# Kernel tuning notes

Hardware: AMD Instinct MI355X
Metric: run time of the kernel (lower is better)

## Reference

```python
import jax, jax.numpy as jnp
import numpy as np

B_SZ, L, D, N = 2, 2048, 1024, 16


def setup_inputs() -> dict:
    key = jax.random.key(0)
    ks = jax.random.split(key, 8)
    x = jax.random.normal(ks[0], (B_SZ, L, D), dtype=jnp.float32)
    # torch.nn.Linear params: weight [out, in], bias [out]; y = x @ W.T + b
    s1 = 1.0 / np.sqrt(D)
    W1 = jax.random.uniform(ks[1], (D, D), minval=-s1, maxval=s1, dtype=jnp.float32)
    b1 = jax.random.uniform(ks[2], (D,), minval=-s1, maxval=s1, dtype=jnp.float32)
    W2 = jax.random.uniform(ks[3], (N, D), minval=-s1, maxval=s1, dtype=jnp.float32)
    b2 = jax.random.uniform(ks[4], (N,), minval=-s1, maxval=s1, dtype=jnp.float32)
    W3 = jax.random.uniform(ks[5], (N, D), minval=-s1, maxval=s1, dtype=jnp.float32)
    b3 = jax.random.uniform(ks[6], (N,), minval=-s1, maxval=s1, dtype=jnp.float32)
    # A: xavier_uniform on (D, N)
    lim = np.sqrt(6.0 / (D + N))
    A = jax.random.uniform(ks[7], (D, N), minval=-lim, maxval=lim, dtype=jnp.float32)
    return {"x": x, "W1": W1, "b1": b1, "W2": W2, "b2": b2, "W3": W3, "b3": b3, "A": A}


def reference(x, W1, b1, W2, b2, W3, b3, A):
    # delta = softplus(fc1(x)); B = fc2(x); C = fc3(x)
    delta = jax.nn.softplus(x @ W1.T + b1)          # [b, l, d]
    Bm = x @ W2.T + b2                               # [b, l, n]
    Cm = x @ W3.T + b3                               # [b, l, n]
    # discretization: dB = einsum('bld,bln->bldn', delta, B)
    dB = jnp.einsum('bld,bln->bldn', delta, Bm)      # [b, l, d, n]
    # dA = exp(einsum('bld,dn->bldn', delta, A)) is computed in the source but
    # multiplies a zero-initialized h, so it does not affect the output.
    # h = dA*0 + x[..., None] * dB
    h = x[..., None] * dB                            # [b, l, d, n]
    y = jnp.einsum('bln,bldn->bld', Cm, h)           # [b, l, d]
    return y
```

## Files before the change

kernel.cpp:

```cpp
#include <hip/hip_runtime.h>
#include <hip/hip_bf16.h>
#include <math.h>


typedef __bf16 bf16x8 __attribute__((ext_vector_type(8)));
typedef __bf16 bf16x4 __attribute__((ext_vector_type(4)));
typedef float  f32x4  __attribute__((ext_vector_type(4)));

#define MDIM 4096
#define KDIM 1024
#define NDIM 1024

__device__ __forceinline__ void async16(const void* g, void* l) {
    __builtin_amdgcn_global_load_lds(
        (const __attribute__((address_space(1))) void*)g,
        (__attribute__((address_space(3))) void*)l, 16, 0, 0);
}

__device__ __forceinline__ float softplus_f(float z) {
    return fmaxf(z, 0.f) + log1pf(__expf(-fabsf(z)));
}

__global__ __launch_bounds__(256)
void prep_kernel(const float* __restrict__ x, const float* __restrict__ W1,
                 const float* __restrict__ W2, const float* __restrict__ b2,
                 const float* __restrict__ W3, const float* __restrict__ b3,
                 __bf16* __restrict__ xb, __bf16* __restrict__ w1b,
                 float* __restrict__ s) {
    __shared__ __align__(16) __bf16 xs[16 * 1032];
    __shared__ float red[4][2][16][16];
    const int t = threadIdx.x;
    const int wave = t >> 6, lane = t & 63;
    const int lrow = lane & 15, quad = lane >> 4;
    const size_t m0 = (size_t)blockIdx.x * 16;

    {
        const float4* src = reinterpret_cast<const float4*>(W1) + (size_t)blockIdx.x * 1024;
        bf16x4* dst = reinterpret_cast<bf16x4*>(w1b) + (size_t)blockIdx.x * 1024;
#pragma unroll
        for (int i = 0; i < 4; ++i) {
            float4 v = src[i * 256 + t];
            bf16x4 h = { (__bf16)v.x, (__bf16)v.y, (__bf16)v.z, (__bf16)v.w };
            dst[i * 256 + t] = h;
        }
    }

#pragma unroll
    for (int i = 0; i < 16; ++i) {
        float4 v = *reinterpret_cast<const float4*>(x + (m0 + i) * KDIM + t * 4);
        bf16x4 h = { (__bf16)v.x, (__bf16)v.y, (__bf16)v.z, (__bf16)v.w };
        *reinterpret_cast<bf16x4*>(&xs[i * 1032 + t * 4]) = h;
        *reinterpret_cast<bf16x4*>(xb + (m0 + i) * KDIM + t * 4) = h;
    }
    __syncthreads();

    f32x4 acc[2] = {};
    const int wk0 = wave * 256;
#pragma unroll
    for (int ks = 0; ks < 256; ks += 32) {
        bf16x8 a = *reinterpret_cast<const bf16x8*>(
            &xs[lrow * 1032 + wk0 + ks + quad * 8]);
        {
            const float* wp = W2 + (size_t)lrow * KDIM + wk0 + ks + quad * 8;
            float4 v0 = *reinterpret_cast<const float4*>(wp);
            float4 v1 = *reinterpret_cast<const float4*>(wp + 4);
            bf16x8 b = { (__bf16)v0.x, (__bf16)v0.y, (__bf16)v0.z, (__bf16)v0.w,
                         (__bf16)v1.x, (__bf16)v1.y, (__bf16)v1.z, (__bf16)v1.w };
            acc[0] = __builtin_amdgcn_mfma_f32_16x16x32_bf16(a, b, acc[0], 0, 0, 0);
        }
        {
            const float* wp = W3 + (size_t)lrow * KDIM + wk0 + ks + quad * 8;
            float4 v0 = *reinterpret_cast<const float4*>(wp);
            float4 v1 = *reinterpret_cast<const float4*>(wp + 4);
            bf16x8 b = { (__bf16)v0.x, (__bf16)v0.y, (__bf16)v0.z, (__bf16)v0.w,
                         (__bf16)v1.x, (__bf16)v1.y, (__bf16)v1.z, (__bf16)v1.w };
            acc[1] = __builtin_amdgcn_mfma_f32_16x16x32_bf16(a, b, acc[1], 0, 0, 0);
        }
    }
#pragma unroll
    for (int r = 0; r < 4; ++r) {
        red[wave][0][quad * 4 + r][lrow] = acc[0][r];
        red[wave][1][quad * 4 + r][lrow] = acc[1][r];
    }
    __syncthreads();

    {
        const int row = t >> 4, n = t & 15;
        float Bv = red[0][0][row][n] + red[1][0][row][n]
                 + red[2][0][row][n] + red[3][0][row][n] + b2[n];
        float Cv = red[0][1][row][n] + red[1][1][row][n]
                 + red[2][1][row][n] + red[3][1][row][n] + b3[n];
        float p = Bv * Cv;
        p += __shfl_xor(p, 1);
        p += __shfl_xor(p, 2);
        p += __shfl_xor(p, 4);
        p += __shfl_xor(p, 8);
        if (n == 0) s[m0 + row] = p;
    }
}

#define GBM 128
#define GBN 64
#define GBK 64
__global__ __launch_bounds__(256)
void gemm_bf(const __bf16* __restrict__ xb, const __bf16* __restrict__ w1b,
             const float* __restrict__ x, const float* __restrict__ b1,
             const float* __restrict__ s, float* __restrict__ y) {
    __shared__ __align__(16) __bf16 As[GBM * GBK];
    __shared__ __align__(16) __bf16 Bs[GBN * GBK];
    const int bm = blockIdx.y, bn = blockIdx.x;
    const int t = threadIdx.x;
    const int wave = t >> 6, lane = t & 63;
    const int wm = (wave >> 1) * 64, wn = (wave & 1) * 32;
    const int lrow = lane & 15, quad = lane >> 4;
    const int srow = lane >> 3;
    const int scol = ((lane & 7) ^ srow) * 8;
    const size_t m0 = (size_t)bm * GBM, n0 = (size_t)bn * GBN;

    f32x4 acc[4][2] = {};

    for (int k0 = 0; k0 < KDIM; k0 += GBK) {
#pragma unroll
        for (int i = 0; i < 4; ++i) {
            int q = i * 4 + wave;
            int row = 8 * q + srow;
            async16(xb + (m0 + row) * KDIM + k0 + scol, &As[q * 512]);
        }
#pragma unroll
        for (int i = 0; i < 2; ++i) {
            int q = i * 4 + wave;
            int row = 8 * q + srow;
            async16(w1b + (n0 + row) * KDIM + k0 + scol, &Bs[q * 512]);
        }
        __syncthreads();

#pragma unroll
        for (int kk = 0; kk < GBK; kk += 32) {
            const int cg = (kk >> 3) + quad;
            bf16x8 af[4], bfr[2];
#pragma unroll
            for (int mi = 0; mi < 4; ++mi) {
                int row = wm + mi * 16 + lrow;
                af[mi] = *reinterpret_cast<const bf16x8*>(
                    &As[row * 64 + ((cg ^ (row & 7)) << 3)]);
            }
#pragma unroll
            for (int ni = 0; ni < 2; ++ni) {
                int row = wn + ni * 16 + lrow;
                bfr[ni] = *reinterpret_cast<const bf16x8*>(
                    &Bs[row * 64 + ((cg ^ (row & 7)) << 3)]);
            }
#pragma unroll
            for (int mi = 0; mi < 4; ++mi)
#pragma unroll
                for (int ni = 0; ni < 2; ++ni)
                    acc[mi][ni] = __builtin_amdgcn_mfma_f32_16x16x32_bf16(
                        af[mi], bfr[ni], acc[mi][ni], 0, 0, 0);
        }
        __syncthreads();
    }

#pragma unroll
    for (int ni = 0; ni < 2; ++ni) {
        const size_t gn = n0 + wn + ni * 16 + lrow;
        const float bias = b1[gn];
#pragma unroll
        for (int mi = 0; mi < 4; ++mi) {
#pragma unroll
            for (int r = 0; r < 4; ++r) {
                const size_t gm = m0 + wm + mi * 16 + quad * 4 + r;
                float z = acc[mi][ni][r] + bias;
                y[gm * NDIM + gn] = x[gm * NDIM + gn] * softplus_f(z) * s[gm];
            }
        }
    }
}

__global__ __launch_bounds__(256)
void s_kernel_fb(const float* __restrict__ x,
                 const float* __restrict__ W2, const float* __restrict__ b2,
                 const float* __restrict__ W3, const float* __restrict__ b3,
                 float* __restrict__ s) {
    __shared__ float xs[1024];
    __shared__ float ps[8][32];
    __shared__ float bc[32];
    const int m = blockIdx.x;
    const int t = threadIdx.x;
    reinterpret_cast<float4*>(xs)[t] =
        reinterpret_cast<const float4*>(x + (size_t)m * 1024)[t];
    __syncthreads();
    const int n = t & 15;
    const int mat = (t >> 4) & 1;
    const int seg = t >> 5;
    const float* __restrict__ W = mat ? W3 : W2;
    const float* __restrict__ wr = W + (size_t)n * 1024 + seg * 128;
    const float* __restrict__ xr = xs + seg * 128;
    float p = 0.f;
#pragma unroll
    for (int i = 0; i < 128; i += 4) {
        float4 w4 = *reinterpret_cast<const float4*>(wr + i);
        float4 x4 = *reinterpret_cast<const float4*>(xr + i);
        p += w4.x * x4.x + w4.y * x4.y + w4.z * x4.z + w4.w * x4.w;
    }
    ps[seg][t & 31] = p;
    __syncthreads();
    if (t < 32) {
        float tot = 0.f;
#pragma unroll
        for (int g = 0; g < 8; ++g) tot += ps[g][t];
        tot += (t < 16) ? b2[t] : b3[t - 16];
        bc[t] = tot;
    }
    __syncthreads();
    if (t == 0) {
        float ss = 0.f;
#pragma unroll
        for (int nn = 0; nn < 16; ++nn) ss += bc[nn] * bc[16 + nn];
        s[m] = ss;
    }
}

#define BM 128
#define BN 64
#define BK 64
#define LDK 72
__global__ __launch_bounds__(256)
void gemm_fused_fb(const float* __restrict__ x, const float* __restrict__ W1,
                   const float* __restrict__ b1, const float* __restrict__ s,
                   float* __restrict__ y) {
    __shared__ __align__(16) __bf16 As[BM * LDK];
    __shared__ __align__(16) __bf16 Bs[BN * LDK];
    const int bm = blockIdx.y;
    const int bn = blockIdx.x;
    const int t = threadIdx.x;
    const int wave = t >> 6;
    const int lane = t & 63;
    const int wm = (wave >> 1) * 64;
    const int wn = (wave & 1) * 32;
    const int lrow = lane & 15;
    const int quad = lane >> 4;
    f32x4 acc[4][2] = {};
    const int rbase = t >> 4;
    const int scol = (t & 15) * 4;
    const float* __restrict__ xg = x + (size_t)(bm * BM) * KDIM + scol;
    const float* __restrict__ wg = W1 + (size_t)(bn * BN) * KDIM + scol;
    for (int k0 = 0; k0 < KDIM; k0 += BK) {
#pragma unroll
        for (int rr = 0; rr < 8; ++rr) {
            int row = rr * 16 + rbase;
            float4 v = *reinterpret_cast<const float4*>(xg + (size_t)row * KDIM + k0);
            bf16x4 h = { (__bf16)v.x, (__bf16)v.y, (__bf16)v.z, (__bf16)v.w };
            *reinterpret_cast<bf16x4*>(&As[row * LDK + scol]) = h;
        }
#pragma unroll
        for (int rr = 0; rr < 4; ++rr) {
            int row = rr * 16 + rbase;
            float4 v = *reinterpret_cast<const float4*>(wg + (size_t)row * KDIM + k0);
            bf16x4 h = { (__bf16)v.x, (__bf16)v.y, (__bf16)v.z, (__bf16)v.w };
            *reinterpret_cast<bf16x4*>(&Bs[row * LDK + scol]) = h;
        }
        __syncthreads();
#pragma unroll
        for (int kk = 0; kk < BK; kk += 32) {
            bf16x8 af[4];
            bf16x8 bfr[2];
#pragma unroll
            for (int mi = 0; mi < 4; ++mi)
                af[mi] = *reinterpret_cast<const bf16x8*>(
                    &As[(wm + mi * 16 + lrow) * LDK + kk + quad * 8]);
#pragma unroll
            for (int ni = 0; ni < 2; ++ni)
                bfr[ni] = *reinterpret_cast<const bf16x8*>(
                    &Bs[(wn + ni * 16 + lrow) * LDK + kk + quad * 8]);
#pragma unroll
            for (int mi = 0; mi < 4; ++mi)
#pragma unroll
                for (int ni = 0; ni < 2; ++ni)
                    acc[mi][ni] = __builtin_amdgcn_mfma_f32_16x16x32_bf16(
                        af[mi], bfr[ni], acc[mi][ni], 0, 0, 0);
        }
        __syncthreads();
    }
    const int gmb = bm * BM + wm;
    const int gnb = bn * BN + wn;
#pragma unroll
    for (int ni = 0; ni < 2; ++ni) {
        const int gn = gnb + ni * 16 + lrow;
        const float bias = b1[gn];
#pragma unroll
        for (int mi = 0; mi < 4; ++mi) {
            const int gm0 = gmb + mi * 16 + quad * 4;
#pragma unroll
            for (int r = 0; r < 4; ++r) {
                const int gm = gm0 + r;
                float z = acc[mi][ni][r] + bias;
                y[(size_t)gm * NDIM + gn] =
                    x[(size_t)gm * NDIM + gn] * softplus_f(z) * s[gm];
            }
        }
    }
}

extern "C" void kernel_launch(void* const* d_in, const int* in_sizes, int n_in,
                              void* d_out, int out_size, void* d_ws, size_t ws_size,
                              hipStream_t stream) {
    const float* x  = (const float*)d_in[0];
    const float* W1 = (const float*)d_in[1];
    const float* b1 = (const float*)d_in[2];
    const float* W2 = (const float*)d_in[3];
    const float* b2 = (const float*)d_in[4];
    const float* W3 = (const float*)d_in[5];
    const float* b3 = (const float*)d_in[6];

    float* y = (float*)d_out;

    const size_t XB_BYTES = (size_t)MDIM * KDIM * 2;
    const size_t WB_BYTES = (size_t)NDIM * KDIM * 2;
    const size_t S_BYTES  = (size_t)MDIM * 4;

    if (ws_size >= XB_BYTES + WB_BYTES + S_BYTES) {
        __bf16* xb  = (__bf16*)d_ws;
        __bf16* w1b = (__bf16*)((char*)d_ws + XB_BYTES);
        float*  s   = (float*)((char*)d_ws + XB_BYTES + WB_BYTES);
        prep_kernel<<<dim3(MDIM / 16), dim3(256), 0, stream>>>(
            x, W1, W2, b2, W3, b3, xb, w1b, s);
        gemm_bf<<<dim3(NDIM / GBN, MDIM / GBM), dim3(256), 0, stream>>>(
            xb, w1b, x, b1, s, y);
    } else {
        float* s = (float*)d_ws;
        s_kernel_fb<<<dim3(MDIM), dim3(256), 0, stream>>>(x, W2, b2, W3, b3, s);
        gemm_fused_fb<<<dim3(NDIM / BN, MDIM / BM), dim3(256), 0, stream>>>(x, W1, b1, s, y);
    }
}
```

Baseline: 114.0 us.

## Stage W2/W3 in LDS for prep; double GEMM K tile and set occupancy hint

In the prep kernel, each wave now loads and converts its slice of W2 and W3 into a padded LDS buffer once, before the MFMA loop. Previously those fp32 weights were fetched and converted inline for every k-step. The GEMM's K tile grows from 64 to 128, which halves the number of barrier-separated iterations, and its XOR swizzle widens to 16 column groups. Launch bounds now request 2 blocks per CU. This raises LDS use per block (about 48KB in the GEMM, plus a large prep buffer) and has no pipelining, so occupancy may drop.

```diff
diff --git a/kernel.cpp b/kernel.cpp
--- a/kernel.cpp
+++ b/kernel.cpp
@@ -28,11 +28,13 @@
                  __bf16* __restrict__ xb, __bf16* __restrict__ w1b,
                  float* __restrict__ s) {
     __shared__ __align__(16) __bf16 xs[16 * 1032];
+    __shared__ __align__(16) __bf16 wq[4][32 * 264];
     __shared__ float red[4][2][16][16];
     const int t = threadIdx.x;
     const int wave = t >> 6, lane = t & 63;
     const int lrow = lane & 15, quad = lane >> 4;
     const size_t m0 = (size_t)blockIdx.x * 16;
+    const int wk0 = wave * 256;
 
     {
         const float4* src = reinterpret_cast<const float4*>(W1) + (size_t)blockIdx.x * 1024;
@@ -52,30 +54,40 @@
         *reinterpret_cast<bf16x4*>(&xs[i * 1032 + t * 4]) = h;
         *reinterpret_cast<bf16x4*>(xb + (m0 + i) * KDIM + t * 4) = h;
     }
+
+    {
+        const int r16  = lane >> 2;
+        const int cseg = (lane & 3) * 64;
+#pragma unroll
+        for (int j = 0; j < 8; ++j) {
+            const int col = cseg + j * 8;
+            const float* p2 = W2 + (size_t)r16 * KDIM + wk0 + col;
+            float4 a0 = *reinterpret_cast<const float4*>(p2);
+            float4 a1 = *reinterpret_cast<const float4*>(p2 + 4);
+            bf16x8 h2 = { (__bf16)a0.x, (__bf16)a0.y, (__bf16)a0.z, (__bf16)a0.w,
+                          (__bf16)a1.x, (__bf16)a1.y, (__bf16)a1.z, (__bf16)a1.w };
+            *reinterpret_cast<bf16x8*>(&wq[wave][r16 * 264 + col]) = h2;
+            const float* p3 = W3 + (size_t)r16 * KDIM + wk0 + col;
+            float4 c0 = *reinterpret_cast<const float4*>(p3);
+            float4 c1 = *reinterpret_cast<const float4*>(p3 + 4);
+            bf16x8 h3 = { (__bf16)c0.x, (__bf16)c0.y, (__bf16)c0.z, (__bf16)c0.w,
+                          (__bf16)c1.x, (__bf16)c1.y, (__bf16)c1.z, (__bf16)c1.w };
+            *reinterpret_cast<bf16x8*>(&wq[wave][(16 + r16) * 264 + col]) = h3;
+        }
+    }
     __syncthreads();
 
     f32x4 acc[2] = {};
-    const int wk0 = wave * 256;
 #pragma unroll
     for (int ks = 0; ks < 256; ks += 32) {
         bf16x8 a = *reinterpret_cast<const bf16x8*>(
             &xs[lrow * 1032 + wk0 + ks + quad * 8]);
-        {
-            const float* wp = W2 + (size_t)lrow * KDIM + wk0 + ks + quad * 8;
-            float4 v0 = *reinterpret_cast<const float4*>(wp);
-            float4 v1 = *reinterpret_cast<const float4*>(wp + 4);
-            bf16x8 b = { (__bf16)v0.x, (__bf16)v0.y, (__bf16)v0.z, (__bf16)v0.w,
-                         (__bf16)v1.x, (__bf16)v1.y, (__bf16)v1.z, (__bf16)v1.w };
-            acc[0] = __builtin_amdgcn_mfma_f32_16x16x32_bf16(a, b, acc[0], 0, 0, 0);
-        }
-        {
-            const float* wp = W3 + (size_t)lrow * KDIM + wk0 + ks + quad * 8;
-            float4 v0 = *reinterpret_cast<const float4*>(wp);
-            float4 v1 = *reinterpret_cast<const float4*>(wp + 4);
-            bf16x8 b = { (__bf16)v0.x, (__bf16)v0.y, (__bf16)v0.z, (__bf16)v0.w,
-                         (__bf16)v1.x, (__bf16)v1.y, (__bf16)v1.z, (__bf16)v1.w };
-            acc[1] = __builtin_amdgcn_mfma_f32_16x16x32_bf16(a, b, acc[1], 0, 0, 0);
-        }
+        bf16x8 b0 = *reinterpret_cast<const bf16x8*>(
+            &wq[wave][lrow * 264 + ks + quad * 8]);
+        acc[0] = __builtin_amdgcn_mfma_f32_16x16x32_bf16(a, b0, acc[0], 0, 0, 0);
+        bf16x8 b1 = *reinterpret_cast<const bf16x8*>(
+            &wq[wave][(16 + lrow) * 264 + ks + quad * 8]);
+        acc[1] = __builtin_amdgcn_mfma_f32_16x16x32_bf16(a, b1, acc[1], 0, 0, 0);
     }
 #pragma unroll
     for (int r = 0; r < 4; ++r) {
@@ -101,8 +113,8 @@
 
 #define GBM 128
 #define GBN 64
-#define GBK 64
-__global__ __launch_bounds__(256)
+#define GBK 128
+__global__ __launch_bounds__(256, 2)
 void gemm_bf(const __bf16* __restrict__ xb, const __bf16* __restrict__ w1b,
              const float* __restrict__ x, const float* __restrict__ b1,
              const float* __restrict__ s, float* __restrict__ y) {
@@ -113,24 +125,26 @@
     const int wave = t >> 6, lane = t & 63;
     const int wm = (wave >> 1) * 64, wn = (wave & 1) * 32;
     const int lrow = lane & 15, quad = lane >> 4;
-    const int srow = lane >> 3;
-    const int scol = ((lane & 7) ^ srow) * 8;
+    const int sr  = lane >> 4;
+    const int pcg = lane & 15;
     const size_t m0 = (size_t)bm * GBM, n0 = (size_t)bn * GBN;
 
     f32x4 acc[4][2] = {};
 
     for (int k0 = 0; k0 < KDIM; k0 += GBK) {
+#pragma unroll
+        for (int i = 0; i < 8; ++i) {
+            int q = i * 4 + wave;
+            int row = q * 4 + sr;
+            int lcg = pcg ^ (row & 15);
+            async16(xb + (m0 + row) * KDIM + k0 + lcg * 8, &As[q * 512]);
+        }
 #pragma unroll
         for (int i = 0; i < 4; ++i) {
             int q = i * 4 + wave;
-            int row = 8 * q + srow;
-            async16(xb + (m0 + row) * KDIM + k0 + scol, &As[q * 512]);
-        }
-#pragma unroll
-        for (int i = 0; i < 2; ++i) {
-            int q = i * 4 + wave;
-            int row = 8 * q + srow;
-            async16(w1b + (n0 + row) * KDIM + k0 + scol, &Bs[q * 512]);
+            int row = q * 4 + sr;
+            int lcg = pcg ^ (row & 15);
+            async16(w1b + (n0 + row) * KDIM + k0 + lcg * 8, &Bs[q * 512]);
         }
         __syncthreads();
 
@@ -142,13 +156,13 @@
             for (int mi = 0; mi < 4; ++mi) {
                 int row = wm + mi * 16 + lrow;
                 af[mi] = *reinterpret_cast<const bf16x8*>(
-                    &As[row * 64 + ((cg ^ (row & 7)) << 3)]);
+                    &As[row * GBK + ((cg ^ (row & 15)) << 3)]);
             }
 #pragma unroll
             for (int ni = 0; ni < 2; ++ni) {
                 int row = wn + ni * 16 + lrow;
                 bfr[ni] = *reinterpret_cast<const bf16x8*>(
-                    &Bs[row * 64 + ((cg ^ (row & 7)) << 3)]);
+                    &Bs[row * GBK + ((cg ^ (row & 15)) << 3)]);
             }
 #pragma unroll
             for (int mi = 0; mi < 4; ++mi)
```

Result: no change. 115.2 us (+1.0%).

## Double-buffer GEMM shared tiles and rewrite prep kernel with fp32 row dot products

Applied to the files above, without the earlier changes.

The main GEMM now uses two shared-memory stages. The next K tile is issued asynchronously while the current one is consumed, which removes one barrier per iteration and overlaps global-to-LDS copies with MFMA work. The prep kernel is restructured to handle 4 rows per block instead of 16. It computes the B and C projections as fp32 dot products with wave shuffles rather than bf16 MFMA, which raises parallelism but means each block rereads the W2/W3 rows. Shared memory for the GEMM doubles, which may reduce occupancy.

```diff
diff --git a/kernel.cpp b/kernel.cpp
--- a/kernel.cpp
+++ b/kernel.cpp
@@ -21,93 +21,95 @@
     return fmaxf(z, 0.f) + log1pf(__expf(-fabsf(z)));
 }
 
+__device__ __forceinline__ float dot4(float4 a, float4 b) {
+    return a.x * b.x + a.y * b.y + a.z * b.z + a.w * b.w;
+}
+
 __global__ __launch_bounds__(256)
-void prep_kernel(const float* __restrict__ x, const float* __restrict__ W1,
-                 const float* __restrict__ W2, const float* __restrict__ b2,
-                 const float* __restrict__ W3, const float* __restrict__ b3,
-                 __bf16* __restrict__ xb, __bf16* __restrict__ w1b,
-                 float* __restrict__ s) {
-    __shared__ __align__(16) __bf16 xs[16 * 1032];
-    __shared__ float red[4][2][16][16];
+void convert_s(const float* __restrict__ x, const float* __restrict__ W1,
+               const float* __restrict__ W2, const float* __restrict__ b2,
+               const float* __restrict__ W3, const float* __restrict__ b3,
+               __bf16* __restrict__ xb, __bf16* __restrict__ w1b,
+               float* __restrict__ s) {
+    __shared__ float xs[4][1024];
+    __shared__ float part[32][4];
     const int t = threadIdx.x;
     const int wave = t >> 6, lane = t & 63;
-    const int lrow = lane & 15, quad = lane >> 4;
-    const size_t m0 = (size_t)blockIdx.x * 16;
+    const size_t m0 = (size_t)blockIdx.x * 4;
 
     {
-        const float4* src = reinterpret_cast<const float4*>(W1) + (size_t)blockIdx.x * 1024;
-        bf16x4* dst = reinterpret_cast<bf16x4*>(w1b) + (size_t)blockIdx.x * 1024;
-#pragma unroll
-        for (int i = 0; i < 4; ++i) {
-            float4 v = src[i * 256 + t];
+        const size_t i = (size_t)blockIdx.x * 256 + t;
+        float4 v = reinterpret_cast<const float4*>(W1)[i];
+        bf16x4 h = { (__bf16)v.x, (__bf16)v.y, (__bf16)v.z, (__bf16)v.w };
+        reinterpret_cast<bf16x4*>(w1b)[i] = h;
+    }
+
+    {
+        const float4* src = reinterpret_cast<const float4*>(x + (m0 + wave) * KDIM);
+        bf16x4* dst = reinterpret_cast<bf16x4*>(xb + (m0 + wave) * KDIM);
+#pragma unroll
+        for (int s4 = 0; s4 < 4; ++s4) {
+            float4 v = src[lane + s4 * 64];
             bf16x4 h = { (__bf16)v.x, (__bf16)v.y, (__bf16)v.z, (__bf16)v.w };
-            dst[i * 256 + t] = h;
-        }
-    }
-
-#pragma unroll
-    for (int i = 0; i < 16; ++i) {
-        float4 v = *reinterpret_cast<const float4*>(x + (m0 + i) * KDIM + t * 4);
-        bf16x4 h = { (__bf16)v.x, (__bf16)v.y, (__bf16)v.z, (__bf16)v.w };
-        *reinterpret_cast<bf16x4*>(&xs[i * 1032 + t * 4]) = h;
-        *reinterpret_cast<bf16x4*>(xb + (m0 + i) * KDIM + t * 4) = h;
-    }
-    __syncthreads();
-
-    f32x4 acc[2] = {};
-    const int wk0 = wave * 256;
-#pragma unroll
-    for (int ks = 0; ks < 256; ks += 32) {
-        bf16x8 a = *reinterpret_cast<const bf16x8*>(
-            &xs[lrow * 1032 + wk0 + ks + quad * 8]);
-        {
-            const float* wp = W2 + (size_t)lrow * KDIM + wk0 + ks + quad * 8;
-            float4 v0 = *reinterpret_cast<const float4*>(wp);
-            float4 v1 = *reinterpret_cast<const float4*>(wp + 4);
-            bf16x8 b = { (__bf16)v0.x, (__bf16)v0.y, (__bf16)v0.z, (__bf16)v0.w,
-                         (__bf16)v1.x, (__bf16)v1.y, (__bf16)v1.z, (__bf16)v1.w };
-            acc[0] = __builtin_amdgcn_mfma_f32_16x16x32_bf16(a, b, acc[0], 0, 0, 0);
-        }
-        {
-            const float* wp = W3 + (size_t)lrow * KDIM + wk0 + ks + quad * 8;
-            float4 v0 = *reinterpret_cast<const float4*>(wp);
-            float4 v1 = *reinterpret_cast<const float4*>(wp + 4);
-            bf16x8 b = { (__bf16)v0.x, (__bf16)v0.y, (__bf16)v0.z, (__bf16)v0.w,
-                         (__bf16)v1.x, (__bf16)v1.y, (__bf16)v1.z, (__bf16)v1.w };
-            acc[1] = __builtin_amdgcn_mfma_f32_16x16x32_bf16(a, b, acc[1], 0, 0, 0);
-        }
-    }
-#pragma unroll
-    for (int r = 0; r < 4; ++r) {
-        red[wave][0][quad * 4 + r][lrow] = acc[0][r];
-        red[wave][1][quad * 4 + r][lrow] = acc[1][r];
-    }
-    __syncthreads();
-
-    {
-        const int row = t >> 4, n = t & 15;
-        float Bv = red[0][0][row][n] + red[1][0][row][n]
-                 + red[2][0][row][n] + red[3][0][row][n] + b2[n];
-        float Cv = red[0][1][row][n] + red[1][1][row][n]
-                 + red[2][1][row][n] + red[3][1][row][n] + b3[n];
-        float p = Bv * Cv;
-        p += __shfl_xor(p, 1);
-        p += __shfl_xor(p, 2);
-        p += __shfl_xor(p, 4);
-        p += __shfl_xor(p, 8);
-        if (n == 0) s[m0 + row] = p;
+            dst[lane + s4 * 64] = h;
+            *reinterpret_cast<float4*>(&xs[wave][(lane + s4 * 64) * 4]) = v;
+        }
+    }
+    __syncthreads();
+
+    float4 X[4][4];
+#pragma unroll
+    for (int r = 0; r < 4; ++r)
+#pragma unroll
+        for (int s4 = 0; s4 < 4; ++s4)
+            X[r][s4] = *reinterpret_cast<const float4*>(&xs[r][(lane + s4 * 64) * 4]);
+
+#pragma unroll
+    for (int wr = 0; wr < 8; ++wr) {
+        const int gr = wave * 8 + wr;
+        const float* __restrict__ Wrow = (gr < 16)
+            ? (W2 + (size_t)gr * KDIM) : (W3 + (size_t)(gr - 16) * KDIM);
+        float4 Wv[4];
+#pragma unroll
+        for (int s4 = 0; s4 < 4; ++s4)
+            Wv[s4] = reinterpret_cast<const float4*>(Wrow)[lane + s4 * 64];
+        float p[4];
+#pragma unroll
+        for (int r = 0; r < 4; ++r) {
+            float a = dot4(Wv[0], X[r][0]) + dot4(Wv[1], X[r][1])
+                    + dot4(Wv[2], X[r][2]) + dot4(Wv[3], X[r][3]);
+#pragma unroll
+            for (int d = 1; d < 64; d <<= 1) a += __shfl_xor(a, d);
+            p[r] = a;
+        }
+        if (lane == 0) {
+            part[gr][0] = p[0]; part[gr][1] = p[1];
+            part[gr][2] = p[2]; part[gr][3] = p[3];
+        }
+    }
+    __syncthreads();
+
+    if (t < 64) {
+        const int r = t >> 4, n = t & 15;
+        float v = (part[n][r] + b2[n]) * (part[n + 16][r] + b3[n]);
+        v += __shfl_xor(v, 1);
+        v += __shfl_xor(v, 2);
+        v += __shfl_xor(v, 4);
+        v += __shfl_xor(v, 8);
+        if (n == 0) s[m0 + r] = v;
     }
 }
 
 #define GBM 128
 #define GBN 64
 #define GBK 64
+#define NIT (KDIM / GBK)
 __global__ __launch_bounds__(256)
 void gemm_bf(const __bf16* __restrict__ xb, const __bf16* __restrict__ w1b,
              const float* __restrict__ x, const float* __restrict__ b1,
              const float* __restrict__ s, float* __restrict__ y) {
-    __shared__ __align__(16) __bf16 As[GBM * GBK];
-    __shared__ __align__(16) __bf16 Bs[GBN * GBK];
+    __shared__ __align__(16) __bf16 As[2][GBM * GBK];
+    __shared__ __align__(16) __bf16 Bs[2][GBN * GBK];
     const int bm = blockIdx.y, bn = blockIdx.x;
     const int t = threadIdx.x;
     const int wave = t >> 6, lane = t & 63;
@@ -119,20 +121,34 @@
 
     f32x4 acc[4][2] = {};
 
-    for (int k0 = 0; k0 < KDIM; k0 += GBK) {
-#pragma unroll
-        for (int i = 0; i < 4; ++i) {
-            int q = i * 4 + wave;
-            int row = 8 * q + srow;
-            async16(xb + (m0 + row) * KDIM + k0 + scol, &As[q * 512]);
-        }
-#pragma unroll
-        for (int i = 0; i < 2; ++i) {
-            int q = i * 4 + wave;
-            int row = 8 * q + srow;
-            async16(w1b + (n0 + row) * KDIM + k0 + scol, &Bs[q * 512]);
-        }
+#pragma unroll
+    for (int i = 0; i < 4; ++i) {
+        int q = i * 4 + wave; int row = 8 * q + srow;
+        async16(xb + (m0 + row) * KDIM + scol, &As[0][q * 512]);
+    }
+#pragma unroll
+    for (int i = 0; i < 2; ++i) {
+        int q = i * 4 + wave; int row = 8 * q + srow;
+        async16(w1b + (n0 + row) * KDIM + scol, &Bs[0][q * 512]);
+    }
+
+    for (int it = 0; it < NIT; ++it) {
+        const int p = it & 1;
         __syncthreads();
+
+        if (it + 1 < NIT) {
+            const int k1 = (it + 1) * GBK;
+#pragma unroll
+            for (int i = 0; i < 4; ++i) {
+                int q = i * 4 + wave; int row = 8 * q + srow;
+                async16(xb + (m0 + row) * KDIM + k1 + scol, &As[p ^ 1][q * 512]);
+            }
+#pragma unroll
+            for (int i = 0; i < 2; ++i) {
+                int q = i * 4 + wave; int row = 8 * q + srow;
+                async16(w1b + (n0 + row) * KDIM + k1 + scol, &Bs[p ^ 1][q * 512]);
+            }
+        }
 
 #pragma unroll
         for (int kk = 0; kk < GBK; kk += 32) {
@@ -142,13 +158,13 @@
             for (int mi = 0; mi < 4; ++mi) {
                 int row = wm + mi * 16 + lrow;
                 af[mi] = *reinterpret_cast<const bf16x8*>(
-                    &As[row * 64 + ((cg ^ (row & 7)) << 3)]);
+                    &As[p][row * GBK + ((cg ^ (row & 7)) << 3)]);
             }
 #pragma unroll
             for (int ni = 0; ni < 2; ++ni) {
                 int row = wn + ni * 16 + lrow;
                 bfr[ni] = *reinterpret_cast<const bf16x8*>(
-                    &Bs[row * 64 + ((cg ^ (row & 7)) << 3)]);
+                    &Bs[p][row * GBK + ((cg ^ (row & 7)) << 3)]);
             }
 #pragma unroll
             for (int mi = 0; mi < 4; ++mi)
@@ -157,7 +173,6 @@
                     acc[mi][ni] = __builtin_amdgcn_mfma_f32_16x16x32_bf16(
                         af[mi], bfr[ni], acc[mi][ni], 0, 0, 0);
         }
-        __syncthreads();
     }
 
 #pragma unroll
@@ -322,7 +337,7 @@
         __bf16* xb  = (__bf16*)d_ws;
         __bf16* w1b = (__bf16*)((char*)d_ws + XB_BYTES);
         float*  s   = (float*)((char*)d_ws + XB_BYTES + WB_BYTES);
-        prep_kernel<<<dim3(MDIM / 16), dim3(256), 0, stream>>>(
+        convert_s<<<dim3(MDIM / 4), dim3(256), 0, stream>>>(
             x, W1, W2, b2, W3, b3, xb, w1b, s);
         gemm_bf<<<dim3(NDIM / GBN, MDIM / GBM), dim3(256), 0, stream>>>(
             xb, w1b, x, b1, s, y);
```

New measurement: 121.3 us. 1.06x slower.

## Fuse B·C row-scale computation into main GEMM and simplify prep to pure conversion

Applied to the files above, without the earlier changes.

The separate prep kernel computed the per-row scale s from fc2/fc3 using MFMA and wrote it to global memory. That kernel is replaced by a flat elementwise bf16 conversion of x, W1 and the stacked W2/W3. The main GEMM now loads a 32-row W2/W3 tile per k-step and accumulates s alongside the fc1 product, reduces it into shared memory, and applies it in the epilogue. This removes the prep GEMM and the s round-trip, but every column block redundantly recomputes s, adding MFMA work and shared-memory traffic.

```diff
diff --git a/kernel.cpp b/kernel.cpp
--- a/kernel.cpp
+++ b/kernel.cpp
@@ -21,93 +21,51 @@
     return fmaxf(z, 0.f) + log1pf(__expf(-fabsf(z)));
 }
 
+#define NX4 ((MDIM * KDIM) / 4)
+#define NW4 ((KDIM * NDIM) / 4)
+#define NC4 ((32 * KDIM) / 4)
 __global__ __launch_bounds__(256)
-void prep_kernel(const float* __restrict__ x, const float* __restrict__ W1,
-                 const float* __restrict__ W2, const float* __restrict__ b2,
-                 const float* __restrict__ W3, const float* __restrict__ b3,
-                 __bf16* __restrict__ xb, __bf16* __restrict__ w1b,
-                 float* __restrict__ s) {
-    __shared__ __align__(16) __bf16 xs[16 * 1032];
-    __shared__ float red[4][2][16][16];
-    const int t = threadIdx.x;
-    const int wave = t >> 6, lane = t & 63;
-    const int lrow = lane & 15, quad = lane >> 4;
-    const size_t m0 = (size_t)blockIdx.x * 16;
-
-    {
-        const float4* src = reinterpret_cast<const float4*>(W1) + (size_t)blockIdx.x * 1024;
-        bf16x4* dst = reinterpret_cast<bf16x4*>(w1b) + (size_t)blockIdx.x * 1024;
-#pragma unroll
-        for (int i = 0; i < 4; ++i) {
-            float4 v = src[i * 256 + t];
+void convert_kernel(const float* __restrict__ x, const float* __restrict__ W1,
+                    const float* __restrict__ W2, const float* __restrict__ W3,
+                    __bf16* __restrict__ xb, __bf16* __restrict__ w1b,
+                    __bf16* __restrict__ wcb) {
+    const size_t i = (size_t)blockIdx.x * 256 + threadIdx.x;
+    if (i < NX4) {
+        float4 v = reinterpret_cast<const float4*>(x)[i];
+        bf16x4 h = { (__bf16)v.x, (__bf16)v.y, (__bf16)v.z, (__bf16)v.w };
+        reinterpret_cast<bf16x4*>(xb)[i] = h;
+    } else if (i < NX4 + NW4) {
+        const size_t j = i - NX4;
+        float4 v = reinterpret_cast<const float4*>(W1)[j];
+        bf16x4 h = { (__bf16)v.x, (__bf16)v.y, (__bf16)v.z, (__bf16)v.w };
+        reinterpret_cast<bf16x4*>(w1b)[j] = h;
+    } else {
+        const size_t j = i - NX4 - NW4;
+        if (j < NC4) {
+            const int row = (int)(j >> 8);
+            const int c4  = (int)(j & 255);
+            const float* __restrict__ src = (row < 16)
+                ? (W2 + (size_t)row * KDIM) : (W3 + (size_t)(row - 16) * KDIM);
+            float4 v = reinterpret_cast<const float4*>(src)[c4];
             bf16x4 h = { (__bf16)v.x, (__bf16)v.y, (__bf16)v.z, (__bf16)v.w };
-            dst[i * 256 + t] = h;
-        }
-    }
-
-#pragma unroll
-    for (int i = 0; i < 16; ++i) {
-        float4 v = *reinterpret_cast<const float4*>(x + (m0 + i) * KDIM + t * 4);
-        bf16x4 h = { (__bf16)v.x, (__bf16)v.y, (__bf16)v.z, (__bf16)v.w };
-        *reinterpret_cast<bf16x4*>(&xs[i * 1032 + t * 4]) = h;
-        *reinterpret_cast<bf16x4*>(xb + (m0 + i) * KDIM + t * 4) = h;
-    }
-    __syncthreads();
-
-    f32x4 acc[2] = {};
-    const int wk0 = wave * 256;
-#pragma unroll
-    for (int ks = 0; ks < 256; ks += 32) {
-        bf16x8 a = *reinterpret_cast<const bf16x8*>(
-            &xs[lrow * 1032 + wk0 + ks + quad * 8]);
-        {
-            const float* wp = W2 + (size_t)lrow * KDIM + wk0 + ks + quad * 8;
-            float4 v0 = *reinterpret_cast<const float4*>(wp);
-            float4 v1 = *reinterpret_cast<const float4*>(wp + 4);
-            bf16x8 b = { (__bf16)v0.x, (__bf16)v0.y, (__bf16)v0.z, (__bf16)v0.w,
-                         (__bf16)v1.x, (__bf16)v1.y, (__bf16)v1.z, (__bf16)v1.w };
-            acc[0] = __builtin_amdgcn_mfma_f32_16x16x32_bf16(a, b, acc[0], 0, 0, 0);
-        }
-        {
-            const float* wp = W3 + (size_t)lrow * KDIM + wk0 + ks + quad * 8;
-            float4 v0 = *reinterpret_cast<const float4*>(wp);
-            float4 v1 = *reinterpret_cast<const float4*>(wp + 4);
-            bf16x8 b = { (__bf16)v0.x, (__bf16)v0.y, (__bf16)v0.z, (__bf16)v0.w,
-                         (__bf16)v1.x, (__bf16)v1.y, (__bf16)v1.z, (__bf16)v1.w };
-            acc[1] = __builtin_amdgcn_mfma_f32_16x16x32_bf16(a, b, acc[1], 0, 0, 0);
-        }
-    }
-#pragma unroll
-    for (int r = 0; r < 4; ++r) {
-        red[wave][0][quad * 4 + r][lrow] = acc[0][r];
-        red[wave][1][quad * 4 + r][lrow] = acc[1][r];
-    }
-    __syncthreads();
-
-    {
-        const int row = t >> 4, n = t & 15;
-        float Bv = red[0][0][row][n] + red[1][0][row][n]
-                 + red[2][0][row][n] + red[3][0][row][n] + b2[n];
-        float Cv = red[0][1][row][n] + red[1][1][row][n]
-                 + red[2][1][row][n] + red[3][1][row][n] + b3[n];
-        float p = Bv * Cv;
-        p += __shfl_xor(p, 1);
-        p += __shfl_xor(p, 2);
-        p += __shfl_xor(p, 4);
-        p += __shfl_xor(p, 8);
-        if (n == 0) s[m0 + row] = p;
-    }
-}
+            reinterpret_cast<bf16x4*>(wcb)[row * 256 + c4] = h;
+        }
+    }
+}
+#define CONV_GRID ((NX4 + NW4 + NC4) / 256)
 
 #define GBM 128
 #define GBN 64
 #define GBK 64
 __global__ __launch_bounds__(256)
 void gemm_bf(const __bf16* __restrict__ xb, const __bf16* __restrict__ w1b,
-             const float* __restrict__ x, const float* __restrict__ b1,
-             const float* __restrict__ s, float* __restrict__ y) {
+             const __bf16* __restrict__ wcb, const float* __restrict__ x,
+             const float* __restrict__ b1, const float* __restrict__ b2,
+             const float* __restrict__ b3, float* __restrict__ y) {
     __shared__ __align__(16) __bf16 As[GBM * GBK];
     __shared__ __align__(16) __bf16 Bs[GBN * GBK];
+    __shared__ __align__(16) __bf16 Ws[32 * GBK];
+    __shared__ float sh_s[GBM];
     const int bm = blockIdx.y, bn = blockIdx.x;
     const int t = threadIdx.x;
     const int wave = t >> 6, lane = t & 63;
@@ -115,40 +73,50 @@
     const int lrow = lane & 15, quad = lane >> 4;
     const int srow = lane >> 3;
     const int scol = ((lane & 7) ^ srow) * 8;
+    const int smi  = (wave & 1) * 2;
     const size_t m0 = (size_t)bm * GBM, n0 = (size_t)bn * GBN;
 
     f32x4 acc[4][2] = {};
+    f32x4 acc_s[2][2] = {};
 
     for (int k0 = 0; k0 < KDIM; k0 += GBK) {
 #pragma unroll
         for (int i = 0; i < 4; ++i) {
-            int q = i * 4 + wave;
-            int row = 8 * q + srow;
+            int q = i * 4 + wave; int row = 8 * q + srow;
             async16(xb + (m0 + row) * KDIM + k0 + scol, &As[q * 512]);
         }
 #pragma unroll
         for (int i = 0; i < 2; ++i) {
-            int q = i * 4 + wave;
-            int row = 8 * q + srow;
+            int q = i * 4 + wave; int row = 8 * q + srow;
             async16(w1b + (n0 + row) * KDIM + k0 + scol, &Bs[q * 512]);
+        }
+        {
+            int row = 8 * wave + srow;
+            async16(wcb + (size_t)row * KDIM + k0 + scol, &Ws[wave * 512]);
         }
         __syncthreads();
 
 #pragma unroll
         for (int kk = 0; kk < GBK; kk += 32) {
             const int cg = (kk >> 3) + quad;
-            bf16x8 af[4], bfr[2];
+            bf16x8 af[4], bfr[2], wf[2];
 #pragma unroll
             for (int mi = 0; mi < 4; ++mi) {
                 int row = wm + mi * 16 + lrow;
                 af[mi] = *reinterpret_cast<const bf16x8*>(
-                    &As[row * 64 + ((cg ^ (row & 7)) << 3)]);
+                    &As[row * GBK + ((cg ^ (row & 7)) << 3)]);
             }
 #pragma unroll
             for (int ni = 0; ni < 2; ++ni) {
                 int row = wn + ni * 16 + lrow;
                 bfr[ni] = *reinterpret_cast<const bf16x8*>(
-                    &Bs[row * 64 + ((cg ^ (row & 7)) << 3)]);
+                    &Bs[row * GBK + ((cg ^ (row & 7)) << 3)]);
+            }
+#pragma unroll
+            for (int nc = 0; nc < 2; ++nc) {
+                int row = nc * 16 + lrow;
+                wf[nc] = *reinterpret_cast<const bf16x8*>(
+                    &Ws[row * GBK + ((cg ^ (row & 7)) << 3)]);
             }
 #pragma unroll
             for (int mi = 0; mi < 4; ++mi)
@@ -156,9 +124,32 @@
                 for (int ni = 0; ni < 2; ++ni)
                     acc[mi][ni] = __builtin_amdgcn_mfma_f32_16x16x32_bf16(
                         af[mi], bfr[ni], acc[mi][ni], 0, 0, 0);
+#pragma unroll
+            for (int i = 0; i < 2; ++i)
+#pragma unroll
+                for (int nc = 0; nc < 2; ++nc)
+                    acc_s[i][nc] = __builtin_amdgcn_mfma_f32_16x16x32_bf16(
+                        af[smi + i], wf[nc], acc_s[i][nc], 0, 0, 0);
         }
         __syncthreads();
     }
+
+    {
+        const float b2v = b2[lrow], b3v = b3[lrow];
+#pragma unroll
+        for (int i = 0; i < 2; ++i) {
+#pragma unroll
+            for (int r = 0; r < 4; ++r) {
+                float p = (acc_s[i][0][r] + b2v) * (acc_s[i][1][r] + b3v);
+                p += __shfl_xor(p, 1);
+                p += __shfl_xor(p, 2);
+                p += __shfl_xor(p, 4);
+                p += __shfl_xor(p, 8);
+                if (lrow == 0) sh_s[wave * 32 + i * 16 + quad * 4 + r] = p;
+            }
+        }
+    }
+    __syncthreads();
 
 #pragma unroll
     for (int ni = 0; ni < 2; ++ni) {
@@ -168,9 +159,10 @@
         for (int mi = 0; mi < 4; ++mi) {
 #pragma unroll
             for (int r = 0; r < 4; ++r) {
-                const size_t gm = m0 + wm + mi * 16 + quad * 4 + r;
+                const int lrowm = wm + mi * 16 + quad * 4 + r;
+                const size_t gm = m0 + lrowm;
                 float z = acc[mi][ni][r] + bias;
-                y[gm * NDIM + gn] = x[gm * NDIM + gn] * softplus_f(z) * s[gm];
+                y[gm * NDIM + gn] = x[gm * NDIM + gn] * softplus_f(z) * sh_s[lrowm];
             }
         }
     }
@@ -316,16 +308,16 @@
 
     const size_t XB_BYTES = (size_t)MDIM * KDIM * 2;
     const size_t WB_BYTES = (size_t)NDIM * KDIM * 2;
-    const size_t S_BYTES  = (size_t)MDIM * 4;
-
-    if (ws_size >= XB_BYTES + WB_BYTES + S_BYTES) {
+    const size_t WC_BYTES = (size_t)32 * KDIM * 2;
+
+    if (ws_size >= XB_BYTES + WB_BYTES + WC_BYTES) {
         __bf16* xb  = (__bf16*)d_ws;
         __bf16* w1b = (__bf16*)((char*)d_ws + XB_BYTES);
-        float*  s   = (float*)((char*)d_ws + XB_BYTES + WB_BYTES);
-        prep_kernel<<<dim3(MDIM / 16), dim3(256), 0, stream>>>(
-            x, W1, W2, b2, W3, b3, xb, w1b, s);
+        __bf16* wcb = (__bf16*)((char*)d_ws + XB_BYTES + WB_BYTES);
+        convert_kernel<<<dim3(CONV_GRID), dim3(256), 0, stream>>>(
+            x, W1, W2, W3, xb, w1b, wcb);
         gemm_bf<<<dim3(NDIM / GBN, MDIM / GBM), dim3(256), 0, stream>>>(
-            xb, w1b, x, b1, s, y);
+            xb, w1b, wcb, x, b1, b2, b3, y);
     } else {
         float* s = (float*)d_ws;
         s_kernel_fb<<<dim3(MDIM), dim3(256), 0, stream>>>(x, W2, b2, W3, b3, s);
```

New measurement: 203.9 us. 1.79x slower.
